# Kernel tuning notes

Measured on AMD Instinct MI355X. Metric: run time of the kernel, lower is better.

## Reference

```python
import jax, jax.numpy as jnp
import numpy as np

N_HIDDEN = 2048
N_HEADS = 64
EXPAND = 2
D_STATE = 128
D_CONV = 4
CHUNK = 128
DT_MIN = 0.001
DT_MAX = 0.1
INNER = EXPAND * N_HIDDEN            # 4096
HEAD_DIM = INNER // N_HEADS          # 64
CONV_DIM = INNER + 2 * D_STATE       # 4352
D_IN_PROJ = 2 * INNER + 2 * D_STATE + N_HEADS  # 8512
EPS = 1e-6


def setup_inputs() -> dict:
    key = jax.random.key(0)
    ks = jax.random.split(key, 10)
    B, L = 2, 2048
    s = lambda fan_in: 1.0 / np.sqrt(fan_in)
    return {
        "x": jax.random.normal(ks[0], (B, L, N_HIDDEN), jnp.float32),
        "W_in": jax.random.normal(ks[1], (N_HIDDEN, D_IN_PROJ), jnp.float32) * s(N_HIDDEN),
        "b_in": jnp.zeros((D_IN_PROJ,), jnp.float32),
        "conv_w": jax.random.normal(ks[2], (D_CONV, 1, CONV_DIM), jnp.float32) * s(D_CONV),
        "conv_b": jnp.zeros((CONV_DIM,), jnp.float32),
        "A_log": jnp.log(jnp.arange(1, N_HEADS + 1, dtype=jnp.float32)),
        "dt_bias": jax.random.normal(ks[3], (N_HEADS,), jnp.float32) * 0.1,
        "D_param": jnp.ones((N_HEADS,), jnp.float32),
        "norm_w": jnp.ones((INNER,), jnp.float32),
        "W_out": jax.random.normal(ks[4], (INNER, N_HIDDEN), jnp.float32) * s(INNER),
        "b_out": jnp.zeros((N_HIDDEN,), jnp.float32),
    }


def _segsum(x):
    t = x.shape[-1]
    cs = jnp.cumsum(x, axis=-1)
    seg = cs[..., :, None] - cs[..., None, :]
    mask = jnp.tril(jnp.ones((t, t), dtype=bool))
    return jnp.where(mask, seg, -jnp.inf)


def _ssd(x, dt, a, b_mat, c_mat, d, dt_bias):
    # x: (B,L,H,P)  dt: (B,L,H)  a: (H,)  b_mat/c_mat: (B,L,H,N)  d: (H,)
    bsz, seq, h, p = x.shape
    dt = jnp.clip(jax.nn.softplus(dt + dt_bias), DT_MIN, DT_MAX)
    d_res = d.reshape(1, 1, h, 1) * x
    x_disc = x * dt[..., None]
    a_disc = a * dt                                   # (B,L,H)
    ch = lambda t_: t_.reshape(bsz, seq // CHUNK, CHUNK, *t_.shape[2:])
    x_blk, b_blk, c_blk = ch(x_disc), ch(b_mat), ch(c_mat)
    a_blk = jnp.transpose(ch(a_disc), (0, 3, 1, 2))   # (B,H,C,Lc)
    a_cum = jnp.cumsum(a_blk, axis=-1)
    l_mat = jnp.exp(_segsum(a_blk))                   # (B,H,C,Lc,Lc)
    y_diag = jnp.einsum("bclhn,bcshn,bhcls,bcshp->bclhp", c_blk, b_blk, l_mat, x_blk)
    decay_states = jnp.exp(a_cum[..., -1:] - a_cum)
    states = jnp.einsum("bclhn,bhcl,bclhp->bchpn", b_blk, decay_states, x_blk)
    states = jnp.concatenate([jnp.zeros_like(states[:, :1]), states], axis=1)
    a_end = jnp.pad(a_cum[..., -1], ((0, 0), (0, 0), (1, 0)))
    decay_chunk = jnp.exp(_segsum(a_end))
    new_states = jnp.einsum("bhzc,bchpn->bzhpn", decay_chunk, states)
    states = new_states[:, :-1]
    y_off = jnp.einsum("bclhn,bchpn,bhcl->bclhp", c_blk, states, jnp.exp(a_cum))
    y = (y_diag + y_off).reshape(bsz, seq, h, p)
    return y + d_res


def reference(x, W_in, b_in, conv_w, conv_b, A_log, dt_bias, D_param, norm_w, W_out, b_out):
    B, L, _ = x.shape
    zxbcdt = x @ W_in + b_in
    z = zxbcdt[..., :INNER]
    xBC = zxbcdt[..., INNER:INNER + CONV_DIM]
    dt = zxbcdt[..., -N_HEADS:]
    # causal depthwise conv1d + silu
    xp = jnp.pad(xBC, ((0, 0), (D_CONV - 1, 0), (0, 0)))
    xBC = jax.lax.conv_general_dilated(
        xp, conv_w, window_strides=(1,), padding="VALID",
        dimension_numbers=("NWC", "WIO", "NWC"), feature_group_count=CONV_DIM,
    ) + conv_b
    xBC = jax.nn.silu(xBC)
    x_ssm = xBC[..., :INNER].reshape(B, L, N_HEADS, HEAD_DIM)
    b_mat = jnp.broadcast_to(xBC[..., INNER:INNER + D_STATE][:, :, None, :], (B, L, N_HEADS, D_STATE))
    c_mat = jnp.broadcast_to(xBC[..., INNER + D_STATE:][:, :, None, :], (B, L, N_HEADS, D_STATE))
    a = -jnp.exp(A_log)
    y = _ssd(x_ssm, dt, a, b_mat, c_mat, D_param, dt_bias)
    y = y.reshape(B, L, INNER)
    # gated RMSNorm
    y = y * jax.nn.silu(z)
    y = y * jax.lax.rsqrt(jnp.mean(y * y, axis=-1, keepdims=True) + EPS) * norm_w
    return y @ W_out + b_out
```

## Files before the change

kernel.cpp:

```cpp
#include <hip/hip_runtime.h>
#include <hip/hip_bf16.h>
#include <cstdint>

typedef __bf16 bf16x8 __attribute__((ext_vector_type(8)));
typedef __bf16 bf16x4 __attribute__((ext_vector_type(4)));
typedef float  f4     __attribute__((ext_vector_type(4)));

constexpr int BATCH   = 2;
constexpr int LSEQ    = 2048;
constexpr int NH      = 2048;
constexpr int INNER   = 4096;
constexpr int DSTATE  = 128;
constexpr int CONVD   = 4352;
constexpr int HEADS   = 64;
constexpr int HDIM    = 64;
constexpr int NPROJ   = 8512;
constexpr int NPROJ_P = 8704;
constexpr int NC      = 16;
constexpr int CH      = 128;
constexpr int ROWS    = BATCH * LSEQ;
constexpr int NBC     = BATCH * NC;

__device__ __forceinline__ f4 f4zero() { f4 v; v.x=0.f; v.y=0.f; v.z=0.f; v.w=0.f; return v; }

__device__ __forceinline__ void gload16(const __bf16* g, const char* l) {
    __builtin_amdgcn_global_load_lds((const __attribute__((address_space(1))) void*)g,
                                     (__attribute__((address_space(3))) void*)l, 16, 0, 0);
}

__global__ __launch_bounds__(256) void k_cast_bf16(const float* __restrict__ in,
                                                   __bf16* __restrict__ out, int n4) {
    int i = blockIdx.x * 256 + threadIdx.x;
    if (i >= n4) return;
    f4 v = ((const f4*)in)[i];
    bf16x4 o;
    o[0] = (__bf16)v.x; o[1] = (__bf16)v.y; o[2] = (__bf16)v.z; o[3] = (__bf16)v.w;
    ((bf16x4*)out)[i] = o;
}

__global__ __launch_bounds__(256) void k_transpose_cast(const float* __restrict__ in,
                                                        __bf16* __restrict__ out,
                                                        int R, int C, int Cp) {
    __shared__ float tile[32][33];
    int bn = blockIdx.x * 32, bk = blockIdx.y * 32;
    int tx = threadIdx.x & 31, ty = threadIdx.x >> 5;
#pragma unroll
    for (int i = 0; i < 4; ++i) {
        int k = bk + ty + i * 8, n = bn + tx;
        tile[ty + i * 8][tx] = (k < R && n < C) ? in[(size_t)k * C + n] : 0.f;
    }
    __syncthreads();
#pragma unroll
    for (int i = 0; i < 4; ++i) {
        int n = bn + ty + i * 8, k = bk + tx;
        if (n < Cp && k < R) out[(size_t)n * R + k] = (__bf16)tile[tx][ty + i * 8];
    }
}

template<int BM, int BN, int WM, int WN, int EPI>
__global__ __launch_bounds__(512, 2) void k_gemm8(
    const __bf16* __restrict__ A, const __bf16* __restrict__ Bt,
    const float* __restrict__ bias, float* __restrict__ Cf,
    __bf16* __restrict__ zf, __bf16* __restrict__ xbcpre, float* __restrict__ dtraw,
    int N, int K, int gridY) {
    extern __shared__ char smem[];
    constexpr int MFRAG = BM / (WM * 16);
    constexpr int NFRAG = BN / (WN * 16);
    constexpr int MH = MFRAG / 2, NH2 = NFRAG / 2;
    constexpr int ALINES = BM / 64, BLINES = BN / 64, LT = ALINES + BLINES;
    constexpr int ABYTES = BM * 128, BUFB = ABYTES + BN * 128;
    constexpr int LPPA = BM / 128, LPPB = BN / 128;

    int tid = threadIdx.x, lane = tid & 63, w = tid >> 6;
    int wm = w / WN, wn = w % WN;

    int bid = blockIdx.x;
    int q = gridDim.x >> 3;
    int wg = (bid & 7) * q + (bid >> 3);
    int bx = wg / gridY, by = wg - bx * gridY;
    int mBase = by * BM, nBase = bx * BN;

    int rl = lane & 15, rq = lane >> 4;
    int kslp = rq ^ (((rl >> 3) & 1) << 1);
    const int rdA = (wm * MFRAG * 16 + rl) * 64 + kslp * 16;
    const int rdB = ABYTES + (wn * NFRAG * 16 + rl) * 64 + kslp * 16;

    int lanep = lane ^ (((lane >> 5) & 1) << 1);
    int srs = lanep >> 2, sksl = lanep & 3;

    const __bf16* sA[ALINES];
#pragma unroll
    for (int li = 0; li < ALINES; ++li)
        sA[li] = A + (size_t)(mBase + (li % LPPA) * 128 + w * 16 + srs) * K + (li / LPPA) * 32 + sksl * 8;
    const __bf16* sB[BLINES];
#pragma unroll
    for (int li = 0; li < BLINES; ++li)
        sB[li] = Bt + (size_t)(nBase + (li % LPPB) * 128 + w * 16 + srs) * K + (li / LPPB) * 32 + sksl * 8;

    auto stage = [&](int buf, int line, int kt) {
        if (line < ALINES) {
            gload16(sA[line] + kt, smem + buf * BUFB + line * 8192 + w * 1024);
        } else {
            int lb = line - ALINES;
            gload16(sB[lb] + kt, smem + buf * BUFB + ABYTES + lb * 8192 + w * 1024);
        }
    };

    f4 acc[MFRAG][NFRAG];
#pragma unroll
    for (int i = 0; i < MFRAG; ++i)
#pragma unroll
        for (int j = 0; j < NFRAG; ++j) acc[i][j] = f4zero();

    const int nt = K >> 6;
#pragma unroll
    for (int li = 0; li < LT; ++li) stage(0, li, 0);
    stage(1, 0, 64);
    stage(1, 1, 64);
    asm volatile("s_waitcnt vmcnt(2)" ::: "memory");
    __builtin_amdgcn_s_barrier();

    for (int t = 0; t < nt; ++t) {
        const int cur = t & 1;
        const int bufoff = cur * BUFB;
        const bool hasNext = (t + 1 < nt);
        const int ktn = (t + 1) << 6;
#pragma unroll
        for (int p = 0; p < 4; ++p) {
            const int mh = p >> 1, nh = p & 1;
            bf16x8 af[MH][2], bv[NH2][2];
#pragma unroll
            for (int mi = 0; mi < MH; ++mi)
#pragma unroll
                for (int ks = 0; ks < 2; ++ks)
                    af[mi][ks] = *(const bf16x8*)(smem + bufoff + ks * (BM * 64) + rdA + (mh * MH + mi) * 1024);
#pragma unroll
            for (int ni = 0; ni < NH2; ++ni)
#pragma unroll
                for (int ks = 0; ks < 2; ++ks)
                    bv[ni][ks] = *(const bf16x8*)(smem + bufoff + ks * (BN * 64) + rdB + (nh * NH2 + ni) * 1024);
            if (hasNext) {
#pragma unroll
                for (int i = 0; i < 3; ++i) {
                    int li = 2 + p * 3 + i;
                    if (li < LT) stage(cur ^ 1, li, ktn);
                }
            }
            __builtin_amdgcn_s_barrier();
            asm volatile("s_waitcnt lgkmcnt(0)" ::: "memory");
            __builtin_amdgcn_sched_barrier(0);
            __builtin_amdgcn_s_setprio(1);
#pragma unroll
            for (int mi = 0; mi < MH; ++mi)
#pragma unroll
                for (int ni = 0; ni < NH2; ++ni)
#pragma unroll
                    for (int ks = 0; ks < 2; ++ks)
                        acc[mh * MH + mi][nh * NH2 + ni] =
                            __builtin_amdgcn_mfma_f32_16x16x32_bf16(af[mi][ks], bv[ni][ks],
                                                                    acc[mh * MH + mi][nh * NH2 + ni], 0, 0, 0);
            __builtin_amdgcn_s_setprio(0);
            __builtin_amdgcn_s_barrier();
        }
        if (t + 2 < nt) {
            stage(cur, 0, (t + 2) << 6);
            stage(cur, 1, (t + 2) << 6);
            asm volatile("s_waitcnt vmcnt(2)" ::: "memory");
            __builtin_amdgcn_s_barrier();
        } else if (hasNext) {
            asm volatile("s_waitcnt vmcnt(0)" ::: "memory");
            __builtin_amdgcn_s_barrier();
        }
    }

    int cl = lane & 15, rq4 = (lane >> 4) * 4;
#pragma unroll
    for (int nf = 0; nf < NFRAG; ++nf) {
        int col0 = nBase + wn * NFRAG * 16 + nf * 16;
        int col = col0 + cl;
        if constexpr (EPI == 1) {
            if (col0 >= NPROJ) continue;
            float bvv = bias[col];
#pragma unroll
            for (int mf = 0; mf < MFRAG; ++mf) {
#pragma unroll
                for (int j = 0; j < 4; ++j) {
                    int row = mBase + wm * MFRAG * 16 + mf * 16 + rq4 + j;
                    float v = acc[mf][nf][j] + bvv;
                    if (col0 < INNER) {
                        zf[(size_t)row * INNER + col] = (__bf16)v;
                    } else if (col0 < INNER + CONVD) {
                        xbcpre[(size_t)row * CONVD + (col - INNER)] = (__bf16)v;
                    } else {
                        dtraw[(size_t)row * HEADS + (col - INNER - CONVD)] = v;
                    }
                }
            }
        } else {
            float bvv = bias[col];
#pragma unroll
            for (int mf = 0; mf < MFRAG; ++mf)
#pragma unroll
                for (int j = 0; j < 4; ++j) {
                    int row = mBase + wm * MFRAG * 16 + mf * 16 + rq4 + j;
                    Cf[(size_t)row * N + col] = acc[mf][nf][j] + bvv;
                }
        }
    }
}

__global__ __launch_bounds__(256) void k_conv_silu(const __bf16* __restrict__ xbcpre,
                                                   const float* __restrict__ conv_w,
                                                   const float* __restrict__ conv_b,
                                                   __bf16* __restrict__ xbc) {
    int idx = blockIdx.x * 256 + threadIdx.x;
    int c8 = idx % (CONVD / 8);
    int bl = idx / (CONVD / 8);
    int l = bl & (LSEQ - 1);
    int c0 = c8 * 8;
    float acc[8];
    const f4* cb4 = (const f4*)(conv_b + c0);
    f4 b0 = cb4[0], b1 = cb4[1];
#pragma unroll
    for (int k = 0; k < 4; ++k) { acc[k] = b0[k]; acc[k + 4] = b1[k]; }
#pragma unroll
    for (int j = 0; j < 4; ++j) {
        int l2 = l + j - 3;
        if (l2 < 0) continue;
        bf16x8 xv = *(const bf16x8*)(xbcpre + (size_t)(bl + j - 3) * CONVD + c0);
        const f4* w4 = (const f4*)(conv_w + j * CONVD + c0);
        f4 w0 = w4[0], w1 = w4[1];
#pragma unroll
        for (int k = 0; k < 4; ++k) {
            acc[k]     += w0[k] * (float)xv[k];
            acc[k + 4] += w1[k] * (float)xv[k + 4];
        }
    }
    bf16x8 o;
#pragma unroll
    for (int k = 0; k < 8; ++k) {
        float a = acc[k];
        o[k] = (__bf16)(a / (1.f + expf(-a)));
    }
    *(bf16x8*)(xbc + (size_t)bl * CONVD + c0) = o;
}

__global__ __launch_bounds__(256) void k_dt(const float* __restrict__ dtraw,
                                            const float* __restrict__ dt_bias,
                                            float* __restrict__ dtp_t) {
    int idx = blockIdx.x * 256 + threadIdx.x;
    int h = idx & 63;
    int bl = idx >> 6;
    int b = bl >> 11, l = bl & (LSEQ - 1);
    float raw = dtraw[idx] + dt_bias[h];
    float sp = raw > 20.f ? raw : log1pf(expf(raw));
    dtp_t[((size_t)(b * HEADS + h)) * LSEQ + l] = fminf(fmaxf(sp, 0.001f), 0.1f);
}

__global__ __launch_bounds__(256) void k_transpose_bc(const __bf16* __restrict__ xbc,
                                                      __bf16* __restrict__ xT,
                                                      __bf16* __restrict__ BtG) {
    int bid = blockIdx.x;
    int ct = bid % 66;
    int rt = (bid / 66) & 1;
    int bc = bid / 132;
    __shared__ float T[64][65];
    int t = threadIdx.x;
    int lr0 = t >> 3, cg = t & 7;
#pragma unroll
    for (int it = 0; it < 2; ++it) {
        int lr = lr0 + it * 32;
        bf16x8 v = *(const bf16x8*)(xbc + (size_t)(bc * CH + rt * 64 + lr) * CONVD + ct * 64 + cg * 8);
#pragma unroll
        for (int j = 0; j < 8; ++j) T[lr][cg * 8 + j] = (float)v[j];
    }
    __syncthreads();
#pragma unroll
    for (int it = 0; it < 2; ++it) {
        int cl = lr0 + it * 32;
        int c = ct * 64 + cl;
        bf16x8 o;
#pragma unroll
        for (int j = 0; j < 8; ++j) o[j] = (__bf16)T[cg * 8 + j][cl];
        __bf16* dst = (c < INNER)
            ? xT  + ((size_t)bc * INNER + c) * CH + rt * 64 + cg * 8
            : BtG + ((size_t)bc * DSTATE + (c - INNER)) * CH + rt * 64 + cg * 8;
        *(bf16x8*)dst = o;
    }
}

__global__ __launch_bounds__(256) void k_cb(const __bf16* __restrict__ xbc,
                                            float* __restrict__ cbT) {
    int bid = blockIdx.x;
    int lg = bid & 7, bc = bid >> 3;
    int tid = threadIdx.x;
    int e0 = lg * 2048 + tid * 8;
    int l = e0 >> 7;
    int s0 = e0 & 127;
    const __bf16* Crow = xbc + (size_t)(bc * CH + l) * CONVD + INNER + DSTATE;
    const __bf16* B0   = xbc + (size_t)(bc * CH + s0) * CONVD + INNER;
    float acc[8];
#pragma unroll
    for (int j = 0; j < 8; ++j) acc[j] = 0.f;
    for (int n8 = 0; n8 < 16; ++n8) {
        bf16x8 cv = *(const bf16x8*)(Crow + n8 * 8);
        float cf[8];
#pragma unroll
        for (int k = 0; k < 8; ++k) cf[k] = (float)cv[k];
#pragma unroll
        for (int j = 0; j < 8; ++j) {
            bf16x8 bvv = *(const bf16x8*)(B0 + (size_t)j * CONVD + n8 * 8);
#pragma unroll
            for (int k = 0; k < 8; ++k) acc[j] += cf[k] * (float)bvv[k];
        }
    }
    float* dst = cbT + ((size_t)bc << 14) + (l << 7) + s0;
#pragma unroll
    for (int j = 0; j < 8; ++j) dst[j] = (s0 + j <= l) ? acc[j] : 0.f;
}

__global__ __launch_bounds__(256) void k_states(const __bf16* __restrict__ xT,
                                                const __bf16* __restrict__ BtG,
                                                const float* __restrict__ dtp_t,
                                                const float* __restrict__ A_log,
                                                __bf16* __restrict__ states,
                                                float* __restrict__ acum_buf,
                                                float* __restrict__ aend_buf) {
    int bid = blockIdx.x;
    int h = bid & 63, c = (bid >> 6) & 15, b = bid >> 10;
    int bc = b * NC + c, bh = b * HEADS + h;
    int tid = threadIdx.x;
    int lane = tid & 63, w = tid >> 6;
    __shared__ __bf16 Ab[64 * 136];
    __shared__ __bf16 Bb[128 * 136];
    __shared__ float s_ac[128], s_dt[128], s_e[128];
    float a_h = -expf(A_log[h]);

    if (tid < 128) {
        float d = dtp_t[(size_t)bh * LSEQ + c * CH + tid];
        s_dt[tid] = d;
        s_ac[tid] = a_h * d;
    }
    __syncthreads();
    for (int offd = 1; offd < 128; offd <<= 1) {
        float v = 0.f;
        if (tid < 128 && tid >= offd) v = s_ac[tid - offd];
        __syncthreads();
        if (tid < 128) s_ac[tid] += v;
        __syncthreads();
    }
    float aend = s_ac[127];
    if (tid < 128) {
        s_e[tid] = expf(aend - s_ac[tid]) * s_dt[tid];
        acum_buf[((size_t)bh * NC + c) * CH + tid] = s_ac[tid];
    }
    if (tid == 0) aend_buf[bh * NC + c] = aend;
    __syncthreads();

    const __bf16* xrow = xT + ((size_t)bc * INNER + h * HDIM) * CH;
#pragma unroll
    for (int it = 0; it < 4; ++it) {
        int task = it * 256 + tid;
        int p = task >> 4, lg2 = task & 15;
        bf16x8 v = *(const bf16x8*)(xrow + (size_t)p * CH + lg2 * 8);
        bf16x8 o;
#pragma unroll
        for (int j = 0; j < 8; ++j) o[j] = (__bf16)((float)v[j] * s_e[lg2 * 8 + j]);
        *(bf16x8*)&Ab[p * 136 + lg2 * 8] = o;
    }
    const __bf16* brow = BtG + (size_t)bc * DSTATE * CH;
#pragma unroll
    for (int it = 0; it < 8; ++it) {
        int task = it * 256 + tid;
        int n = task >> 4, lg2 = task & 15;
        *(bf16x8*)&Bb[n * 136 + lg2 * 8] = *(const bf16x8*)(brow + (size_t)n * CH + lg2 * 8);
    }
    __syncthreads();

    int rl = lane & 15, kq = (lane >> 4) * 8, rq = lane >> 4;
    f4 acc[8];
#pragma unroll
    for (int i = 0; i < 8; ++i) acc[i] = f4zero();
#pragma unroll
    for (int ks = 0; ks < 4; ++ks) {
        int k0 = ks * 32;
        bf16x8 a = *(const bf16x8*)&Ab[(w * 16 + rl) * 136 + k0 + kq];
#pragma unroll
        for (int nf = 0; nf < 8; ++nf) {
            bf16x8 bfr = *(const bf16x8*)&Bb[(nf * 16 + rl) * 136 + k0 + kq];
            acc[nf] = __builtin_amdgcn_mfma_f32_16x16x32_bf16(a, bfr, acc[nf], 0, 0, 0);
        }
    }
    __syncthreads();
#pragma unroll
    for (int nf = 0; nf < 8; ++nf)
#pragma unroll
        for (int j = 0; j < 4; ++j)
            Ab[(w * 16 + rq * 4 + j) * 136 + nf * 16 + rl] = (__bf16)acc[nf][j];
    __syncthreads();
    __bf16* sbase = states + ((size_t)(bc * HEADS + h)) * (HDIM * DSTATE);
#pragma unroll
    for (int it = 0; it < 4; ++it) {
        int task = it * 256 + tid;
        int p = task >> 4, ng = task & 15;
        *(bf16x8*)(sbase + (size_t)p * DSTATE + ng * 8) = *(const bf16x8*)&Ab[p * 136 + ng * 8];
    }
}

__global__ __launch_bounds__(128) void k_scan(__bf16* __restrict__ states,
                                              const float* __restrict__ aend_buf) {
    int s = blockIdx.x & 7;
    int bh = blockIdx.x >> 3;
    int b = bh >> 6, h = bh & 63;
    int tid = threadIdx.x;
    size_t off = (size_t)s * 1024 + (size_t)tid * 8;
    float run[8];
#pragma unroll
    for (int j = 0; j < 8; ++j) run[j] = 0.f;
    for (int c = 0; c < NC; ++c) {
        float dec = expf(aend_buf[bh * NC + c]);
        __bf16* base = states + ((size_t)((b * NC + c) * HEADS + h)) * (HDIM * DSTATE) + off;
        bf16x8 sv = *(bf16x8*)base;
        bf16x8 o;
#pragma unroll
        for (int j = 0; j < 8; ++j) o[j] = (__bf16)run[j];
        *(bf16x8*)base = o;
#pragma unroll
        for (int j = 0; j < 8; ++j) run[j] = run[j] * dec + (float)sv[j];
    }
}

__global__ __launch_bounds__(256) void k_out(const __bf16* __restrict__ xbc,
                                             const __bf16* __restrict__ xT,
                                             const float* __restrict__ dtp_t,
                                             const float* __restrict__ cbT,
                                             const __bf16* __restrict__ prev,
                                             const float* __restrict__ acum_buf,
                                             const float* __restrict__ D_param,
                                             __bf16* __restrict__ ybuf) {
    int bid = blockIdx.x;
    int h = bid & 63, c = (bid >> 6) & 15, b = bid >> 10;
    int bc = b * NC + c, bh = b * HEADS + h;
    int tid = threadIdx.x;
    int lane = tid & 63, w = tid >> 6;
    __shared__ __bf16 Ab[128 * 136];
    __shared__ __bf16 Bb[64 * 136];
    __shared__ float s_ac[128], s_dt[128];
    if (tid < 128) {
        s_ac[tid] = acum_buf[((size_t)bh * NC + c) * CH + tid];
        s_dt[tid] = dtp_t[(size_t)bh * LSEQ + c * CH + tid];
    }

#pragma unroll
    for (int it = 0; it < 8; ++it) {
        int task = it * 256 + tid;
        int l = task >> 4, ng = task & 15;
        *(bf16x8*)&Ab[l * 136 + ng * 8] =
            *(const bf16x8*)(xbc + (size_t)(bc * CH + l) * CONVD + INNER + DSTATE + ng * 8);
    }
    const __bf16* pbase = prev + ((size_t)(bc * HEADS + h)) * (HDIM * DSTATE);
#pragma unroll
    for (int it = 0; it < 4; ++it) {
        int task = it * 256 + tid;
        int p = task >> 4, ng = task & 15;
        *(bf16x8*)&Bb[p * 136 + ng * 8] = *(const bf16x8*)(pbase + (size_t)p * DSTATE + ng * 8);
    }
    __syncthreads();

    int rl = lane & 15, kq = (lane >> 4) * 8, rq = lane >> 4;
    f4 acc[2][4];
#pragma unroll
    for (int i = 0; i < 2; ++i)
#pragma unroll
        for (int j = 0; j < 4; ++j) acc[i][j] = f4zero();

#pragma unroll
    for (int ks = 0; ks < 4; ++ks) {
        int k0 = ks * 32;
        bf16x8 a0 = *(const bf16x8*)&Ab[(w * 32 + rl) * 136 + k0 + kq];
        bf16x8 a1 = *(const bf16x8*)&Ab[(w * 32 + 16 + rl) * 136 + k0 + kq];
#pragma unroll
        for (int nf = 0; nf < 4; ++nf) {
            bf16x8 bfr = *(const bf16x8*)&Bb[(nf * 16 + rl) * 136 + k0 + kq];
            acc[0][nf] = __builtin_amdgcn_mfma_f32_16x16x32_bf16(a0, bfr, acc[0][nf], 0, 0, 0);
            acc[1][nf] = __builtin_amdgcn_mfma_f32_16x16x32_bf16(a1, bfr, acc[1][nf], 0, 0, 0);
        }
    }
#pragma unroll
    for (int mf = 0; mf < 2; ++mf)
#pragma unroll
        for (int j = 0; j < 4; ++j) {
            float el = expf(s_ac[w * 32 + mf * 16 + rq * 4 + j]);
#pragma unroll
            for (int nf = 0; nf < 4; ++nf) acc[mf][nf][j] *= el;
        }
    __syncthreads();

    const float* cbb = cbT + ((size_t)bc << 14);
#pragma unroll
    for (int it = 0; it < 8; ++it) {
        int task = it * 256 + tid;
        int l = task >> 4, sg = task & 15;
        int s0 = sg * 8;
        const f4* cv4 = (const f4*)(cbb + (l << 7) + s0);
        f4 c0 = cv4[0], c1 = cv4[1];
        float acl = s_ac[l];
        bf16x8 o;
#pragma unroll
        for (int j = 0; j < 8; ++j) {
            int s = s0 + j;
            float cj = (j < 4) ? c0[j] : c1[j - 4];
            float m = 0.f;
            if (s <= l) m = cj * expf(acl - s_ac[s]) * s_dt[s];
            o[j] = (__bf16)m;
        }
        *(bf16x8*)&Ab[l * 136 + s0] = o;
    }
    const __bf16* xrow = xT + ((size_t)bc * INNER + h * HDIM) * CH;
#pragma unroll
    for (int it = 0; it < 4; ++it) {
        int task = it * 256 + tid;
        int p = task >> 4, lg2 = task & 15;
        *(bf16x8*)&Bb[p * 136 + lg2 * 8] = *(const bf16x8*)(xrow + (size_t)p * CH + lg2 * 8);
    }
    __syncthreads();

#pragma unroll
    for (int ks = 0; ks < 4; ++ks) {
        int k0 = ks * 32;
        bf16x8 a0 = *(const bf16x8*)&Ab[(w * 32 + rl) * 136 + k0 + kq];
        bf16x8 a1 = *(const bf16x8*)&Ab[(w * 32 + 16 + rl) * 136 + k0 + kq];
#pragma unroll
        for (int nf = 0; nf < 4; ++nf) {
            bf16x8 bfr = *(const bf16x8*)&Bb[(nf * 16 + rl) * 136 + k0 + kq];
            acc[0][nf] = __builtin_amdgcn_mfma_f32_16x16x32_bf16(a0, bfr, acc[0][nf], 0, 0, 0);
            acc[1][nf] = __builtin_amdgcn_mfma_f32_16x16x32_bf16(a1, bfr, acc[1][nf], 0, 0, 0);
        }
    }
    __syncthreads();

    float* yT = (float*)Ab;
#pragma unroll
    for (int mf = 0; mf < 2; ++mf)
#pragma unroll
        for (int nf = 0; nf < 4; ++nf)
#pragma unroll
            for (int j = 0; j < 4; ++j)
                yT[(w * 32 + mf * 16 + rq * 4 + j) * 68 + nf * 16 + rl] = acc[mf][nf][j];
    __syncthreads();

    float dh = D_param[h];
#pragma unroll
    for (int it = 0; it < 4; ++it) {
        int task = it * 256 + tid;
        int l = task >> 3, pg = task & 7;
        const f4* yv4 = (const f4*)&yT[l * 68 + pg * 8];
        f4 y0 = yv4[0], y1 = yv4[1];
        bf16x8 xv = *(const bf16x8*)(xbc + (size_t)(bc * CH + l) * CONVD + h * HDIM + pg * 8);
        bf16x8 o;
#pragma unroll
        for (int j = 0; j < 4; ++j) {
            o[j]     = (__bf16)(y0[j] + dh * (float)xv[j]);
            o[j + 4] = (__bf16)(y1[j] + dh * (float)xv[j + 4]);
        }
        *(bf16x8*)(ybuf + (size_t)(bc * CH + l) * INNER + h * HDIM + pg * 8) = o;
    }
}

__global__ __launch_bounds__(256) void k_gate_norm(__bf16* __restrict__ ybuf,
                                                   const __bf16* __restrict__ zf,
                                                   const float* __restrict__ norm_w) {
    int row = blockIdx.x, tid = threadIdx.x;
    bf16x8* yrow = (bf16x8*)(ybuf + (size_t)row * INNER);
    const bf16x8* zrow = (const bf16x8*)(zf + (size_t)row * INNER);
    float v[2][8];
    float ss = 0.f;
#pragma unroll
    for (int i = 0; i < 2; ++i) {
        bf16x8 yv = yrow[i * 256 + tid];
        bf16x8 zv = zrow[i * 256 + tid];
#pragma unroll
        for (int j = 0; j < 8; ++j) {
            float z = (float)zv[j];
            float t = (float)yv[j] * (z / (1.f + expf(-z)));
            v[i][j] = t;
            ss += t * t;
        }
    }
#pragma unroll
    for (int off = 32; off > 0; off >>= 1) ss += __shfl_down(ss, off, 64);
    __shared__ float red[4];
    __shared__ float scs;
    if ((tid & 63) == 0) red[tid >> 6] = ss;
    __syncthreads();
    if (tid == 0) scs = rsqrtf((red[0] + red[1] + red[2] + red[3]) * (1.f / INNER) + 1e-6f);
    __syncthreads();
    float scale = scs;
#pragma unroll
    for (int i = 0; i < 2; ++i) {
        const f4* nw = (const f4*)(norm_w + (i * 256 + tid) * 8);
        f4 w0 = nw[0], w1 = nw[1];
        bf16x8 o;
#pragma unroll
        for (int j = 0; j < 4; ++j) {
            o[j]     = (__bf16)(v[i][j]     * scale * w0[j]);
            o[j + 4] = (__bf16)(v[i][j + 4] * scale * w1[j]);
        }
        yrow[i * 256 + tid] = o;
    }
}

extern "C" void kernel_launch(void* const* d_in, const int* in_sizes, int n_in,
                              void* d_out, int out_size, void* d_ws, size_t ws_size,
                              hipStream_t stream) {
    const float* x       = (const float*)d_in[0];
    const float* W_in    = (const float*)d_in[1];
    const float* b_in    = (const float*)d_in[2];
    const float* conv_w  = (const float*)d_in[3];
    const float* conv_b  = (const float*)d_in[4];
    const float* A_log   = (const float*)d_in[5];
    const float* dt_bias = (const float*)d_in[6];
    const float* D_par   = (const float*)d_in[7];
    const float* norm_w  = (const float*)d_in[8];
    const float* W_out   = (const float*)d_in[9];
    const float* b_out   = (const float*)d_in[10];
    float* out = (float*)d_out;

    char* ws = (char*)d_ws;
    constexpr size_t SZ_XBF    = (size_t)ROWS * NH * 2;
    constexpr size_t SZ_WTIN   = (size_t)NPROJ_P * NH * 2;
    constexpr size_t SZ_R1     = SZ_XBF + SZ_WTIN;
    constexpr size_t SZ_ZF     = (size_t)ROWS * INNER * 2;
    constexpr size_t SZ_XBC    = (size_t)ROWS * CONVD * 2;
    constexpr size_t SZ_STATES = (size_t)NBC * HEADS * HDIM * DSTATE * 2;
    constexpr size_t SZ_CBT    = (size_t)NBC * CH * CH * 4;
    constexpr size_t SZ_ACUM   = (size_t)BATCH * HEADS * NC * CH * 4;
    constexpr size_t SZ_AEND   = (size_t)BATCH * HEADS * NC * 4;
    constexpr size_t SZ_DTP    = (size_t)ROWS * HEADS * 4;

    __bf16* xbf    = (__bf16*)(ws);
    __bf16* wtin   = (__bf16*)(ws + SZ_XBF);
    __bf16* zf     = (__bf16*)(ws + SZ_R1);
    __bf16* xbcpre = (__bf16*)(ws + SZ_R1 + SZ_ZF);
    __bf16* xbc    = (__bf16*)(ws + SZ_R1 + SZ_ZF + SZ_XBC);
    float*  dtraw  = (float*) (ws + SZ_R1 + SZ_ZF + 2 * SZ_XBC);
    __bf16* states = (__bf16*)(ws);
    float*  cbT    = (float*) (ws + SZ_STATES);
    float*  acum   = (float*) (ws + SZ_STATES + SZ_CBT);
    float*  aend   = (float*) (ws + SZ_STATES + SZ_CBT + SZ_ACUM);
    float*  dtp_t  = (float*) (ws + SZ_STATES + SZ_CBT + SZ_ACUM + SZ_AEND);
    __bf16* BtG    = (__bf16*)(ws + SZ_STATES + SZ_CBT + SZ_ACUM + SZ_AEND + SZ_DTP);
    __bf16* ybuf   = xbcpre;
    __bf16* wtout  = xbc;
    __bf16* xT     = (__bf16*)out;

    (void)ws_size; (void)in_sizes; (void)n_in; (void)out_size;

    hipFuncSetAttribute(reinterpret_cast<const void*>(&k_gemm8<256,256,2,4,1>),
                        hipFuncAttributeMaxDynamicSharedMemorySize, 131072);
    hipFuncSetAttribute(reinterpret_cast<const void*>(&k_gemm8<256,128,4,2,0>),
                        hipFuncAttributeMaxDynamicSharedMemorySize, 98304);

    k_cast_bf16<<<(ROWS * NH / 4 + 255) / 256, 256, 0, stream>>>(x, xbf, ROWS * NH / 4);
    k_transpose_cast<<<dim3(NPROJ_P / 32, NH / 32), 256, 0, stream>>>(W_in, wtin, NH, NPROJ, NPROJ_P);

    k_gemm8<256,256,2,4,1><<<(NPROJ_P / 256) * (ROWS / 256), 512, 131072, stream>>>(
        xbf, wtin, b_in, nullptr, zf, xbcpre, dtraw, NPROJ_P, NH, ROWS / 256);

    k_conv_silu<<<ROWS * (CONVD / 8) / 256, 256, 0, stream>>>(xbcpre, conv_w, conv_b, xbc);
    k_dt<<<ROWS * HEADS / 256, 256, 0, stream>>>(dtraw, dt_bias, dtp_t);
    k_transpose_bc<<<NBC * 132, 256, 0, stream>>>(xbc, xT, BtG);
    k_cb<<<NBC * 8, 256, 0, stream>>>(xbc, cbT);
    k_states<<<NBC * HEADS, 256, 0, stream>>>(xT, BtG, dtp_t, A_log, states, acum, aend);
    k_scan<<<BATCH * HEADS * 8, 128, 0, stream>>>(states, aend);
    k_out<<<NBC * HEADS, 256, 0, stream>>>(xbc, xT, dtp_t, cbT, states, acum, D_par, ybuf);
    k_gate_norm<<<ROWS, 256, 0, stream>>>(ybuf, zf, norm_w);

    k_transpose_cast<<<dim3(NH / 32, INNER / 32), 256, 0, stream>>>(W_out, wtout, INNER, NH, NH);
    k_gemm8<256,128,4,2,0><<<(NH / 128) * (ROWS / 256), 512, 98304, stream>>>(
        ybuf, wtout, b_out, out, nullptr, nullptr, nullptr, NH, INNER, ROWS / 256);
}
```

Baseline: 531.3 us.

## Restructure GEMM main loop into register double-buffered half-K software pipeline

The bf16 MFMA GEMM main loop now splits each 64-wide K tile into two k-slices. The LDS fragments for the next slice are loaded into a second register set while MFMAs run on the current one, so the four per-tile phases and most of their barriers go away. Global-to-LDS staging is regrouped to match: the first four lines are prefetched two tiles ahead and the rest one tile ahead, with adjusted vmcnt waits. This is meant to hide LDS read latency behind MFMA work and cut synchronization, at the cost of more VGPRs for the duplicated fragment registers under 512-thread, 2-block launch bounds.

```diff
diff --git a/kernel.cpp b/kernel.cpp
--- a/kernel.cpp
+++ b/kernel.cpp
@@ -66,7 +66,6 @@
     extern __shared__ char smem[];
     constexpr int MFRAG = BM / (WM * 16);
     constexpr int NFRAG = BN / (WN * 16);
-    constexpr int MH = MFRAG / 2, NH2 = NFRAG / 2;
     constexpr int ALINES = BM / 64, BLINES = BN / 64, LT = ALINES + BLINES;
     constexpr int ABYTES = BM * 128, BUFB = ABYTES + BN * 128;
     constexpr int LPPA = BM / 128, LPPB = BN / 128;
@@ -106,70 +105,68 @@
         }
     };
 
+    bf16x8 a0[MFRAG], b0[NFRAG], a1[MFRAG], b1[NFRAG];
+    auto ldregs = [&](int bufoff, int ks, bf16x8* ar, bf16x8* br) {
+#pragma unroll
+        for (int i = 0; i < MFRAG; ++i)
+            ar[i] = *(const bf16x8*)(smem + bufoff + ks * (BM * 64) + rdA + i * 1024);
+#pragma unroll
+        for (int i = 0; i < NFRAG; ++i)
+            br[i] = *(const bf16x8*)(smem + bufoff + ks * (BN * 64) + rdB + i * 1024);
+    };
+
     f4 acc[MFRAG][NFRAG];
 #pragma unroll
     for (int i = 0; i < MFRAG; ++i)
 #pragma unroll
         for (int j = 0; j < NFRAG; ++j) acc[i][j] = f4zero();
 
+    auto domfma = [&](bf16x8* ar, bf16x8* br) {
+        __builtin_amdgcn_s_setprio(1);
+#pragma unroll
+        for (int mi = 0; mi < MFRAG; ++mi)
+#pragma unroll
+            for (int ni = 0; ni < NFRAG; ++ni)
+                acc[mi][ni] = __builtin_amdgcn_mfma_f32_16x16x32_bf16(ar[mi], br[ni], acc[mi][ni], 0, 0, 0);
+        __builtin_amdgcn_s_setprio(0);
+    };
+
     const int nt = K >> 6;
 #pragma unroll
     for (int li = 0; li < LT; ++li) stage(0, li, 0);
-    stage(1, 0, 64);
-    stage(1, 1, 64);
-    asm volatile("s_waitcnt vmcnt(2)" ::: "memory");
+#pragma unroll
+    for (int li = 0; li < 4; ++li) stage(1, li, 64);
+    asm volatile("s_waitcnt vmcnt(4)" ::: "memory");
     __builtin_amdgcn_s_barrier();
+    ldregs(0, 0, a0, b0);
 
     for (int t = 0; t < nt; ++t) {
         const int cur = t & 1;
         const int bufoff = cur * BUFB;
-        const bool hasNext = (t + 1 < nt);
-        const int ktn = (t + 1) << 6;
-#pragma unroll
-        for (int p = 0; p < 4; ++p) {
-            const int mh = p >> 1, nh = p & 1;
-            bf16x8 af[MH][2], bv[NH2][2];
-#pragma unroll
-            for (int mi = 0; mi < MH; ++mi)
-#pragma unroll
-                for (int ks = 0; ks < 2; ++ks)
-                    af[mi][ks] = *(const bf16x8*)(smem + bufoff + ks * (BM * 64) + rdA + (mh * MH + mi) * 1024);
-#pragma unroll
-            for (int ni = 0; ni < NH2; ++ni)
-#pragma unroll
-                for (int ks = 0; ks < 2; ++ks)
-                    bv[ni][ks] = *(const bf16x8*)(smem + bufoff + ks * (BN * 64) + rdB + (nh * NH2 + ni) * 1024);
-            if (hasNext) {
-#pragma unroll
-                for (int i = 0; i < 3; ++i) {
-                    int li = 2 + p * 3 + i;
-                    if (li < LT) stage(cur ^ 1, li, ktn);
-                }
+        ldregs(bufoff, 1, a1, b1);
+        if (t + 1 < nt) {
+#pragma unroll
+            for (int li = 4; li < LT; ++li) stage(cur ^ 1, li, (t + 1) << 6);
+        }
+        __builtin_amdgcn_sched_barrier(0);
+        domfma(a0, b0);
+        asm volatile("s_waitcnt lgkmcnt(0)" ::: "memory");
+        __builtin_amdgcn_sched_barrier(0);
+        __builtin_amdgcn_s_barrier();
+        if (t + 2 < nt) {
+#pragma unroll
+            for (int li = 0; li < 4; ++li) stage(cur, li, (t + 2) << 6);
+        }
+        __builtin_amdgcn_sched_barrier(0);
+        domfma(a1, b1);
+        if (t + 1 < nt) {
+            if (t + 2 < nt) {
+                asm volatile("s_waitcnt vmcnt(4)" ::: "memory");
+            } else {
+                asm volatile("s_waitcnt vmcnt(0)" ::: "memory");
             }
             __builtin_amdgcn_s_barrier();
-            asm volatile("s_waitcnt lgkmcnt(0)" ::: "memory");
-            __builtin_amdgcn_sched_barrier(0);
-            __builtin_amdgcn_s_setprio(1);
-#pragma unroll
-            for (int mi = 0; mi < MH; ++mi)
-#pragma unroll
-                for (int ni = 0; ni < NH2; ++ni)
-#pragma unroll
-                    for (int ks = 0; ks < 2; ++ks)
-                        acc[mh * MH + mi][nh * NH2 + ni] =
-                            __builtin_amdgcn_mfma_f32_16x16x32_bf16(af[mi][ks], bv[ni][ks],
-                                                                    acc[mh * MH + mi][nh * NH2 + ni], 0, 0, 0);
-            __builtin_amdgcn_s_setprio(0);
-            __builtin_amdgcn_s_barrier();
-        }
-        if (t + 2 < nt) {
-            stage(cur, 0, (t + 2) << 6);
-            stage(cur, 1, (t + 2) << 6);
-            asm volatile("s_waitcnt vmcnt(2)" ::: "memory");
-            __builtin_amdgcn_s_barrier();
-        } else if (hasNext) {
-            asm volatile("s_waitcnt vmcnt(0)" ::: "memory");
-            __builtin_amdgcn_s_barrier();
+            ldregs((cur ^ 1) * BUFB, 0, a0, b0);
         }
     }
 
```

Result: faster. 460.3 us (-13.4%).
